# Kernel optimization log

Hardware: AMD Instinct MI355X
Metric: run time of the kernel (lower is better)

Reference implementation:

```python
import jax, jax.numpy as jnp
from jax import lax
import numpy as np

B, D, L = 32, 64, 4096
E = 8          # num_experts
K = 2          # top-k
OC = 32        # out_channels


def setup_inputs() -> dict:
    key = jax.random.key(0)
    ks = jax.random.split(key, 6)
    x = jax.random.normal(ks[0], (B, D, L), dtype=jnp.float32)
    # gating weight [D*5, E] (torch init is zeros; use small random for a meaningful reference)
    w_gate = jax.random.normal(ks[1], (D * 5, E), dtype=jnp.float32) * 0.02
    # Conv1d(D -> OC, kernel 3)
    conv1_w = jax.random.normal(ks[2], (OC, D, 3), dtype=jnp.float32) * (1.0 / np.sqrt(D * 3))
    conv1_b = jax.random.normal(ks[3], (OC,), dtype=jnp.float32) * 0.01
    # Conv1d(OC -> OC*E, kernel 1)
    conv2_w = jax.random.normal(ks[4], (OC * E, OC, 1), dtype=jnp.float32) * (1.0 / np.sqrt(OC))
    conv2_b = jax.random.normal(ks[5], (OC * E,), dtype=jnp.float32) * 0.01
    return {"x": x, "w_gate": w_gate, "conv1_w": conv1_w, "conv1_b": conv1_b,
            "conv2_w": conv2_w, "conv2_b": conv2_b}


def _gates(g_in, w_gate):
    # eval-mode noisy_top_k_gating: no noise, softmax -> top-(k+1) -> renormalize top-k -> scatter
    logits = jax.nn.softmax(g_in @ w_gate, axis=1)            # [B, E]
    top_v, top_i = lax.top_k(logits, min(K + 1, E))           # sorted descending
    vk = top_v[:, :K]
    ik = top_i[:, :K]
    gk = vk / (jnp.sum(vk, axis=1, keepdims=True) + 1e-6)
    gates = jnp.zeros_like(logits).at[jnp.arange(logits.shape[0])[:, None], ik].set(gk)
    return gates


def reference(x, w_gate, conv1_w, conv1_b, conv2_w, conv2_b):
    b, d, l = x.shape
    g_in = x[:, :, -6:-1].reshape(b, d * 5)                   # last-5-timestep gating features
    gates = _gates(g_in, w_gate)                              # [B, E]
    dn = ("NCH", "OIH", "NCH")
    h = lax.conv_general_dilated(x, conv1_w, (1,), "VALID", dimension_numbers=dn)
    h = jnp.tanh(h + conv1_b[None, :, None])                  # [B, OC, L-2]
    out = lax.conv_general_dilated(h, conv2_w, (1,), "VALID", dimension_numbers=dn)
    out = out + conv2_b[None, :, None]                        # [B, OC*E, L']
    lp = out.shape[-1]
    out = out.transpose(0, 2, 1).reshape(b, lp, OC, E)        # [B, L', OC, E]
    moe = jnp.einsum("blde,be->bld", out, gates)              # weighted combine
    return moe.transpose(0, 2, 1)                             # [B, OC, L']
```

## Files before the change

### kernel.cpp

```cpp
#include <hip/hip_runtime.h>
#include <math.h>

#define B_  32
#define D_  64
#define L_  4096
#define E_  8
#define OC_ 32
#define LP_ 4094
#define TILE 128
#define NT   32

typedef __attribute__((ext_vector_type(8)))  short short8;
typedef __attribute__((ext_vector_type(16))) float float16;

static __device__ __forceinline__ unsigned short f2bf(float f) {
    unsigned u = __float_as_uint(f);
    return (unsigned short)((u + 0x7fffu + ((u >> 16) & 1u)) >> 16);
}
static __device__ __forceinline__ unsigned cvtpk(float a, float b) {
    unsigned r;
    asm("v_cvt_pk_bf16_f32 %0, %1, %2" : "=v"(r) : "v"(a), "v"(b));
    return r;
}
static __device__ __forceinline__ float fast_tanh(float x) {
    float e = __expf(2.0f * x);
    return fmaf(-2.0f, __builtin_amdgcn_rcpf(e + 1.0f), 1.0f);
}


__global__ __launch_bounds__(256)
void prep_kernel(const float* __restrict__ x,
                 const float* __restrict__ w_gate,
                 const float* __restrict__ c1w,
                 const float* __restrict__ c2w,
                 const float* __restrict__ c2b,
                 float* __restrict__ beff,
                 unsigned short* __restrict__ aF,
                 unsigned short* __restrict__ wf2)
{
    const int tid = threadIdx.x;

    if (blockIdx.x == 8) {
        for (int i = tid; i < 12 * 64 * 8; i += 256) {
            int ks = i >> 9, lane = (i >> 3) & 63, ii = i & 7;
            int oc = lane & 31, half = lane >> 5;
            int kp = ks * 16 + half * 8 + ii;
            int t = kp >> 6, c = kp & 63;
            aF[i] = f2bf(c1w[oc * 192 + c * 3 + t]);
        }
        return;
    }

    const int wv = tid >> 6, lane = tid & 63;
    const int b  = blockIdx.x * 4 + wv;
    const int d  = lane;

    float xv[5];
    #pragma unroll
    for (int t = 0; t < 5; ++t)
        xv[t] = x[((size_t)b * D_ + d) * L_ + (L_ - 6) + t];

    float part[E_];
    #pragma unroll
    for (int e = 0; e < E_; ++e) part[e] = 0.f;
    #pragma unroll
    for (int t = 0; t < 5; ++t) {
        const float* wg = w_gate + (d * 5 + t) * E_;
        #pragma unroll
        for (int e = 0; e < E_; ++e) part[e] += xv[t] * wg[e];
    }
    #pragma unroll
    for (int off = 1; off < 64; off <<= 1) {
        #pragma unroll
        for (int e = 0; e < E_; ++e)
            part[e] += __shfl_xor(part[e], off, 64);
    }
    float m = part[0];
    #pragma unroll
    for (int e = 1; e < E_; ++e) m = fmaxf(m, part[e]);
    float p[E_], s = 0.f;
    #pragma unroll
    for (int e = 0; e < E_; ++e) { p[e] = expf(part[e] - m); s += p[e]; }
    float inv = 1.f / s;
    #pragma unroll
    for (int e = 0; e < E_; ++e) p[e] *= inv;

    int i0 = 0;
    #pragma unroll
    for (int e = 1; e < E_; ++e) if (p[e] > p[i0]) i0 = e;
    int i1 = (i0 == 0) ? 1 : 0;
    #pragma unroll
    for (int e = 0; e < E_; ++e) {
        if (e == i0) continue;
        if (p[e] > p[i1]) i1 = e;
    }
    const float v0 = p[i0], v1 = p[i1];
    const float den = v0 + v1 + 1e-6f;
    const float g0 = v0 / den, g1 = v1 / den;

    {
        const int dd = lane & 31, half = lane >> 5;
        #pragma unroll
        for (int ks = 0; ks < 2; ++ks) {
            #pragma unroll
            for (int i = 0; i < 8; ++i) {
                int oc = ks * 16 + half * 8 + i;
                float v = g0 * c2w[(dd * E_ + i0) * OC_ + oc]
                        + g1 * c2w[(dd * E_ + i1) * OC_ + oc];
                wf2[((b * 2 + ks) * 64 + lane) * 8 + i] = f2bf(v);
            }
        }
    }
    if (d < OC_)
        beff[b * OC_ + d] = g0 * c2b[d * E_ + i0] + g1 * c2b[d * E_ + i1];
}

__global__ __launch_bounds__(256, 4)
void fused_main(const float* __restrict__ x,
                const unsigned short* __restrict__ aF,
                const unsigned short* __restrict__ wf2,
                const float* __restrict__ beff,
                const float* __restrict__ c1b,
                float* __restrict__ out)
{
    __shared__ __align__(16) unsigned short xT[130 * 64];

    const int tid  = threadIdx.x;
    const int lane = tid & 63;
    const int wv   = tid >> 6;
    const int b    = blockIdx.x >> 5;
    const int l0   = (blockIdx.x & 31) << 7;
    const float* xb = x + (size_t)b * (D_ * L_);

    {
        const int c2 = tid >> 3;
        const int jb = (tid & 7) << 2;
        const float* p0 = xb + (size_t)(2 * c2) * L_ + l0;
        const float* p1 = p0 + L_;
        #pragma unroll
        for (int jq = 0; jq < 4; ++jq) {
            int j = jq * 32 + jb;
            float4 v0 = *(const float4*)(p0 + j);
            float4 v1 = *(const float4*)(p1 + j);
            float e0[4] = {v0.x, v0.y, v0.z, v0.w};
            float e1[4] = {v1.x, v1.y, v1.z, v1.w};
            #pragma unroll
            for (int r = 0; r < 4; ++r) {
                int row = j + r;
                int off = (row * 128 + c2 * 4) ^ ((row & 7) << 4);
                *(unsigned*)((char*)xT + off) = cvtpk(e0[r], e1[r]);
            }
        }
        if (tid < 64) {
            int cc2 = tid >> 1, jj = tid & 1;
            int row = TILE + jj;
            int lg  = l0 + row;
            float f0 = 0.f, f1 = 0.f;
            if (lg < L_) {
                f0 = xb[(size_t)(2 * cc2) * L_ + lg];
                f1 = xb[(size_t)(2 * cc2 + 1) * L_ + lg];
            }
            int off = (row * 128 + cc2 * 4) ^ ((row & 7) << 4);
            *(unsigned*)((char*)xT + off) = cvtpk(f0, f1);
        }
    }

    const int cl = lane & 31;
    const int hi = lane >> 5;

    __syncthreads();

    const int cb = wv * 32;
    float16 acc = (float16)0.0f;
    #pragma unroll
    for (int t = 0; t < 3; ++t) {
        int row = cb + cl + t;
        int rb  = row * 128;
        int swz = (row & 7) << 4;
        #pragma unroll
        for (int q = 0; q < 4; ++q) {
            short8 af = *(const short8*)(aF + ((t * 4 + q) * 64 + lane) * 8);
            int off = (rb + q * 32 + hi * 16) ^ swz;
            short8 bf = *(const short8*)((const char*)xT + off);
            acc = __builtin_amdgcn_mfma_f32_32x32x16_bf16(af, bf, acc, 0, 0, 0);
        }
    }

    short8 a2[2];
    a2[0] = *(const short8*)(wf2 + ((b * 2 + 0) * 64 + lane) * 8);
    a2[1] = *(const short8*)(wf2 + ((b * 2 + 1) * 64 + lane) * 8);

    float th[16];
    #pragma unroll
    for (int r = 0; r < 16; ++r) {
        int row = (r & 3) + 8 * (r >> 2) + 4 * hi;
        th[r] = fast_tanh(acc[r] + c1b[row]);
    }

    unsigned x0a = hi ? cvtpk(th[0],  th[1])  : cvtpk(th[4],  th[5]);
    unsigned x0b = hi ? cvtpk(th[2],  th[3])  : cvtpk(th[6],  th[7]);
    unsigned x1a = hi ? cvtpk(th[8],  th[9])  : cvtpk(th[12], th[13]);
    unsigned x1b = hi ? cvtpk(th[10], th[11]) : cvtpk(th[14], th[15]);
    unsigned r0a = (unsigned)__shfl_xor((int)x0a, 32, 64);
    unsigned r0b = (unsigned)__shfl_xor((int)x0b, 32, 64);
    unsigned r1a = (unsigned)__shfl_xor((int)x1a, 32, 64);
    unsigned r1b = (unsigned)__shfl_xor((int)x1b, 32, 64);

    union U { short8 s8; unsigned u[4]; };
    U b0, b1;
    b0.u[0] = hi ? r0a : cvtpk(th[0], th[1]);
    b0.u[1] = hi ? r0b : cvtpk(th[2], th[3]);
    b0.u[2] = hi ? cvtpk(th[4], th[5]) : r0a;
    b0.u[3] = hi ? cvtpk(th[6], th[7]) : r0b;
    b1.u[0] = hi ? r1a : cvtpk(th[8], th[9]);
    b1.u[1] = hi ? r1b : cvtpk(th[10], th[11]);
    b1.u[2] = hi ? cvtpk(th[12], th[13]) : r1a;
    b1.u[3] = hi ? cvtpk(th[14], th[15]) : r1b;

    float16 acc2 = (float16)0.0f;
    acc2 = __builtin_amdgcn_mfma_f32_32x32x16_bf16(a2[0], b0.s8, acc2, 0, 0, 0);
    acc2 = __builtin_amdgcn_mfma_f32_32x32x16_bf16(a2[1], b1.s8, acc2, 0, 0, 0);

    int l = l0 + cb + cl;
    if (l < LP_) {
        const float* be = beff + b * OC_;
        float* ob = out + (size_t)b * (OC_ * (size_t)LP_) + l;
        #pragma unroll
        for (int r = 0; r < 16; ++r) {
            int row = (r & 3) + 8 * (r >> 2) + 4 * hi;
            ob[(size_t)row * LP_] = acc2[r] + be[row];
        }
    }
}

extern "C" void kernel_launch(void* const* d_in, const int* in_sizes, int n_in,
                              void* d_out, int out_size, void* d_ws, size_t ws_size,
                              hipStream_t stream)
{
    const float* x      = (const float*)d_in[0];
    const float* w_gate = (const float*)d_in[1];
    const float* c1w    = (const float*)d_in[2];
    const float* c1b    = (const float*)d_in[3];
    const float* c2w    = (const float*)d_in[4];
    const float* c2b    = (const float*)d_in[5];
    float* out = (float*)d_out;

    char* ws = (char*)d_ws;
    float* beff         = (float*)ws;
    unsigned short* aF  = (unsigned short*)(ws + 4096);
    unsigned short* wf2 = (unsigned short*)(ws + 16384);

    prep_kernel<<<9, 256, 0, stream>>>(x, w_gate, c1w, c2w, c2b, beff, aF, wf2);
    fused_main<<<B_ * NT, 256, 0, stream>>>(x, aF, wf2, beff, c1b, out);
}
```

Before: 22.00 us.

## Fuse gating and weight-prep kernel into main conv kernel

Removes the separate prep kernel and recomputes, in every block, the gating softmax/top-k, the bf16 packing of conv1 weights into LDS, and the gate-combined conv2 weights and bias. This eliminates one kernel launch and the serialized dependency between the two kernels. In exchange, each of the 1024 blocks redundantly does gating reductions and extra global loads of weights, which adds per-block latency before the MFMA work.

```diff
diff --git a/kernel.cpp b/kernel.cpp
--- a/kernel.cpp
+++ b/kernel.cpp
@@ -13,10 +13,6 @@
 typedef __attribute__((ext_vector_type(8)))  short short8;
 typedef __attribute__((ext_vector_type(16))) float float16;
 
-static __device__ __forceinline__ unsigned short f2bf(float f) {
-    unsigned u = __float_as_uint(f);
-    return (unsigned short)((u + 0x7fffu + ((u >> 16) & 1u)) >> 16);
-}
 static __device__ __forceinline__ unsigned cvtpk(float a, float b) {
     unsigned r;
     asm("v_cvt_pk_bf16_f32 %0, %1, %2" : "=v"(r) : "v"(a), "v"(b));
@@ -27,103 +23,17 @@
     return fmaf(-2.0f, __builtin_amdgcn_rcpf(e + 1.0f), 1.0f);
 }
 
-
-__global__ __launch_bounds__(256)
-void prep_kernel(const float* __restrict__ x,
-                 const float* __restrict__ w_gate,
-                 const float* __restrict__ c1w,
-                 const float* __restrict__ c2w,
-                 const float* __restrict__ c2b,
-                 float* __restrict__ beff,
-                 unsigned short* __restrict__ aF,
-                 unsigned short* __restrict__ wf2)
-{
-    const int tid = threadIdx.x;
-
-    if (blockIdx.x == 8) {
-        for (int i = tid; i < 12 * 64 * 8; i += 256) {
-            int ks = i >> 9, lane = (i >> 3) & 63, ii = i & 7;
-            int oc = lane & 31, half = lane >> 5;
-            int kp = ks * 16 + half * 8 + ii;
-            int t = kp >> 6, c = kp & 63;
-            aF[i] = f2bf(c1w[oc * 192 + c * 3 + t]);
-        }
-        return;
-    }
-
-    const int wv = tid >> 6, lane = tid & 63;
-    const int b  = blockIdx.x * 4 + wv;
-    const int d  = lane;
-
-    float xv[5];
-    #pragma unroll
-    for (int t = 0; t < 5; ++t)
-        xv[t] = x[((size_t)b * D_ + d) * L_ + (L_ - 6) + t];
-
-    float part[E_];
-    #pragma unroll
-    for (int e = 0; e < E_; ++e) part[e] = 0.f;
-    #pragma unroll
-    for (int t = 0; t < 5; ++t) {
-        const float* wg = w_gate + (d * 5 + t) * E_;
-        #pragma unroll
-        for (int e = 0; e < E_; ++e) part[e] += xv[t] * wg[e];
-    }
-    #pragma unroll
-    for (int off = 1; off < 64; off <<= 1) {
-        #pragma unroll
-        for (int e = 0; e < E_; ++e)
-            part[e] += __shfl_xor(part[e], off, 64);
-    }
-    float m = part[0];
-    #pragma unroll
-    for (int e = 1; e < E_; ++e) m = fmaxf(m, part[e]);
-    float p[E_], s = 0.f;
-    #pragma unroll
-    for (int e = 0; e < E_; ++e) { p[e] = expf(part[e] - m); s += p[e]; }
-    float inv = 1.f / s;
-    #pragma unroll
-    for (int e = 0; e < E_; ++e) p[e] *= inv;
-
-    int i0 = 0;
-    #pragma unroll
-    for (int e = 1; e < E_; ++e) if (p[e] > p[i0]) i0 = e;
-    int i1 = (i0 == 0) ? 1 : 0;
-    #pragma unroll
-    for (int e = 0; e < E_; ++e) {
-        if (e == i0) continue;
-        if (p[e] > p[i1]) i1 = e;
-    }
-    const float v0 = p[i0], v1 = p[i1];
-    const float den = v0 + v1 + 1e-6f;
-    const float g0 = v0 / den, g1 = v1 / den;
-
-    {
-        const int dd = lane & 31, half = lane >> 5;
-        #pragma unroll
-        for (int ks = 0; ks < 2; ++ks) {
-            #pragma unroll
-            for (int i = 0; i < 8; ++i) {
-                int oc = ks * 16 + half * 8 + i;
-                float v = g0 * c2w[(dd * E_ + i0) * OC_ + oc]
-                        + g1 * c2w[(dd * E_ + i1) * OC_ + oc];
-                wf2[((b * 2 + ks) * 64 + lane) * 8 + i] = f2bf(v);
-            }
-        }
-    }
-    if (d < OC_)
-        beff[b * OC_ + d] = g0 * c2b[d * E_ + i0] + g1 * c2b[d * E_ + i1];
-}
-
 __global__ __launch_bounds__(256, 4)
-void fused_main(const float* __restrict__ x,
-                const unsigned short* __restrict__ aF,
-                const unsigned short* __restrict__ wf2,
-                const float* __restrict__ beff,
-                const float* __restrict__ c1b,
-                float* __restrict__ out)
+void fused_all(const float* __restrict__ x,
+               const float* __restrict__ w_gate,
+               const float* __restrict__ c1w,
+               const float* __restrict__ c1b,
+               const float* __restrict__ c2w,
+               const float* __restrict__ c2b,
+               float* __restrict__ out)
 {
     __shared__ __align__(16) unsigned short xT[130 * 64];
+    __shared__ __align__(16) unsigned short aFl[12 * 64 * 8];
 
     const int tid  = threadIdx.x;
     const int lane = tid & 63;
@@ -165,8 +75,97 @@
         }
     }
 
+    {
+        const int oc = tid >> 3;
+        const int c0 = (tid & 7) << 3;
+        const float* wp = c1w + oc * 192 + c0 * 3;
+        float v[24];
+        #pragma unroll
+        for (int q = 0; q < 6; ++q)
+            *(float4*)(v + 4 * q) = *(const float4*)(wp + 4 * q);
+        const int ksoff = c0 >> 4;
+        const int half  = (c0 >> 3) & 1;
+        #pragma unroll
+        for (int t = 0; t < 3; ++t) {
+            union { short8 s8; unsigned u[4]; } w8;
+            #pragma unroll
+            for (int jj = 0; jj < 4; ++jj)
+                w8.u[jj] = cvtpk(v[(2 * jj) * 3 + t], v[(2 * jj + 1) * 3 + t]);
+            int base = ((t * 4 + ksoff) * 64 + half * 32 + oc) * 8;
+            *(short8*)(aFl + base) = w8.s8;
+        }
+    }
+
+    int i0, i1;
+    float g0, g1;
+    {
+        const int d = lane;
+        float part[E_];
+        #pragma unroll
+        for (int e = 0; e < E_; ++e) part[e] = 0.f;
+        #pragma unroll
+        for (int t = 0; t < 5; ++t) {
+            float xvt = xb[(size_t)d * L_ + (L_ - 6) + t];
+            const float* wgp = w_gate + (d * 5 + t) * E_;
+            float4 wa = *(const float4*)wgp;
+            float4 wb = *(const float4*)(wgp + 4);
+            part[0] = fmaf(xvt, wa.x, part[0]);
+            part[1] = fmaf(xvt, wa.y, part[1]);
+            part[2] = fmaf(xvt, wa.z, part[2]);
+            part[3] = fmaf(xvt, wa.w, part[3]);
+            part[4] = fmaf(xvt, wb.x, part[4]);
+            part[5] = fmaf(xvt, wb.y, part[5]);
+            part[6] = fmaf(xvt, wb.z, part[6]);
+            part[7] = fmaf(xvt, wb.w, part[7]);
+        }
+        #pragma unroll
+        for (int off = 1; off < 64; off <<= 1) {
+            #pragma unroll
+            for (int e = 0; e < E_; ++e)
+                part[e] += __shfl_xor(part[e], off, 64);
+        }
+        float m = part[0];
+        #pragma unroll
+        for (int e = 1; e < E_; ++e) m = fmaxf(m, part[e]);
+        float p[E_], s = 0.f;
+        #pragma unroll
+        for (int e = 0; e < E_; ++e) { p[e] = expf(part[e] - m); s += p[e]; }
+        float inv = 1.f / s;
+        #pragma unroll
+        for (int e = 0; e < E_; ++e) p[e] *= inv;
+
+        i0 = 0;
+        #pragma unroll
+        for (int e = 1; e < E_; ++e) if (p[e] > p[i0]) i0 = e;
+        i1 = (i0 == 0) ? 1 : 0;
+        #pragma unroll
+        for (int e = 0; e < E_; ++e) {
+            if (e == i0) continue;
+            if (p[e] > p[i1]) i1 = e;
+        }
+        const float v0 = p[i0], v1 = p[i1];
+        const float den = v0 + v1 + 1e-6f;
+        g0 = v0 / den;
+        g1 = v1 / den;
+    }
+
     const int cl = lane & 31;
     const int hi = lane >> 5;
+
+    short8 a2[2];
+    #pragma unroll
+    for (int ks = 0; ks < 2; ++ks) {
+        const float* q0 = c2w + (cl * E_ + i0) * OC_ + ks * 16 + hi * 8;
+        const float* q1 = c2w + (cl * E_ + i1) * OC_ + ks * 16 + hi * 8;
+        float4 u0a = *(const float4*)q0, u0b = *(const float4*)(q0 + 4);
+        float4 u1a = *(const float4*)q1, u1b = *(const float4*)(q1 + 4);
+        union { short8 s8; unsigned u[4]; } f;
+        f.u[0] = cvtpk(fmaf(g0, u0a.x, g1 * u1a.x), fmaf(g0, u0a.y, g1 * u1a.y));
+        f.u[1] = cvtpk(fmaf(g0, u0a.z, g1 * u1a.z), fmaf(g0, u0a.w, g1 * u1a.w));
+        f.u[2] = cvtpk(fmaf(g0, u0b.x, g1 * u1b.x), fmaf(g0, u0b.y, g1 * u1b.y));
+        f.u[3] = cvtpk(fmaf(g0, u0b.z, g1 * u1b.z), fmaf(g0, u0b.w, g1 * u1b.w));
+        a2[ks] = f.s8;
+    }
 
     __syncthreads();
 
@@ -179,16 +178,12 @@
         int swz = (row & 7) << 4;
         #pragma unroll
         for (int q = 0; q < 4; ++q) {
-            short8 af = *(const short8*)(aF + ((t * 4 + q) * 64 + lane) * 8);
+            short8 af = *(const short8*)(aFl + ((t * 4 + q) * 64 + lane) * 8);
             int off = (rb + q * 32 + hi * 16) ^ swz;
             short8 bf = *(const short8*)((const char*)xT + off);
             acc = __builtin_amdgcn_mfma_f32_32x32x16_bf16(af, bf, acc, 0, 0, 0);
         }
     }
-
-    short8 a2[2];
-    a2[0] = *(const short8*)(wf2 + ((b * 2 + 0) * 64 + lane) * 8);
-    a2[1] = *(const short8*)(wf2 + ((b * 2 + 1) * 64 + lane) * 8);
 
     float th[16];
     #pragma unroll
@@ -223,12 +218,12 @@
 
     int l = l0 + cb + cl;
     if (l < LP_) {
-        const float* be = beff + b * OC_;
         float* ob = out + (size_t)b * (OC_ * (size_t)LP_) + l;
         #pragma unroll
         for (int r = 0; r < 16; ++r) {
             int row = (r & 3) + 8 * (r >> 2) + 4 * hi;
-            ob[(size_t)row * LP_] = acc2[r] + be[row];
+            float bb = fmaf(g0, c2b[row * E_ + i0], g1 * c2b[row * E_ + i1]);
+            ob[(size_t)row * LP_] = acc2[r] + bb;
         }
     }
 }
@@ -245,11 +240,5 @@
     const float* c2b    = (const float*)d_in[5];
     float* out = (float*)d_out;
 
-    char* ws = (char*)d_ws;
-    float* beff         = (float*)ws;
-    unsigned short* aF  = (unsigned short*)(ws + 4096);
-    unsigned short* wf2 = (unsigned short*)(ws + 16384);
-
-    prep_kernel<<<9, 256, 0, stream>>>(x, w_gate, c1w, c2w, c2b, beff, aF, wf2);
-    fused_main<<<B_ * NT, 256, 0, stream>>>(x, aF, wf2, beff, c1b, out);
-}
+    fused_all<<<B_ * NT, 256, 0, stream>>>(x, w_gate, c1w, c1b, c2w, c2b, out);
+}
```

After: 22.75 us. +3.4%, slower.

## Load conv input fragments directly from global memory, drop LDS staging

Applied to the files above, without the earlier changes.

The shared-memory transpose tile and its barrier are removed. Each lane now reads its eight channels at three consecutive positions straight from global memory into registers, packs them to bf16 and feeds the MFMAs. This avoids LDS writes and reads and the block-wide sync, at the cost of scalar, less vectorised global loads. Adjacent lanes read overlapping addresses, so the design relies on caches to absorb the threefold reuse. Positions near the end are clamped rather than zero-padded, and the affected outputs are masked at the store.

```diff
diff --git a/kernel.cpp b/kernel.cpp
--- a/kernel.cpp
+++ b/kernel.cpp
@@ -123,8 +123,6 @@
                 const float* __restrict__ c1b,
                 float* __restrict__ out)
 {
-    __shared__ __align__(16) unsigned short xT[130 * 64];
-
     const int tid  = threadIdx.x;
     const int lane = tid & 63;
     const int wv   = tid >> 6;
@@ -132,58 +130,38 @@
     const int l0   = (blockIdx.x & 31) << 7;
     const float* xb = x + (size_t)b * (D_ * L_);
 
-    {
-        const int c2 = tid >> 3;
-        const int jb = (tid & 7) << 2;
-        const float* p0 = xb + (size_t)(2 * c2) * L_ + l0;
-        const float* p1 = p0 + L_;
-        #pragma unroll
-        for (int jq = 0; jq < 4; ++jq) {
-            int j = jq * 32 + jb;
-            float4 v0 = *(const float4*)(p0 + j);
-            float4 v1 = *(const float4*)(p1 + j);
-            float e0[4] = {v0.x, v0.y, v0.z, v0.w};
-            float e1[4] = {v1.x, v1.y, v1.z, v1.w};
-            #pragma unroll
-            for (int r = 0; r < 4; ++r) {
-                int row = j + r;
-                int off = (row * 128 + c2 * 4) ^ ((row & 7) << 4);
-                *(unsigned*)((char*)xT + off) = cvtpk(e0[r], e1[r]);
-            }
-        }
-        if (tid < 64) {
-            int cc2 = tid >> 1, jj = tid & 1;
-            int row = TILE + jj;
-            int lg  = l0 + row;
-            float f0 = 0.f, f1 = 0.f;
-            if (lg < L_) {
-                f0 = xb[(size_t)(2 * cc2) * L_ + lg];
-                f1 = xb[(size_t)(2 * cc2 + 1) * L_ + lg];
-            }
-            int off = (row * 128 + cc2 * 4) ^ ((row & 7) << 4);
-            *(unsigned*)((char*)xT + off) = cvtpk(f0, f1);
-        }
-    }
-
     const int cl = lane & 31;
     const int hi = lane >> 5;
-
-    __syncthreads();
-
     const int cb = wv * 32;
+
+    const int l  = l0 + cb + cl;
+    const int lc = (l > L_ - 3) ? (L_ - 3) : l;
+
     float16 acc = (float16)0.0f;
     #pragma unroll
-    for (int t = 0; t < 3; ++t) {
-        int row = cb + cl + t;
-        int rb  = row * 128;
-        int swz = (row & 7) << 4;
-        #pragma unroll
-        for (int q = 0; q < 4; ++q) {
-            short8 af = *(const short8*)(aF + ((t * 4 + q) * 64 + lane) * 8);
-            int off = (rb + q * 32 + hi * 16) ^ swz;
-            short8 bf = *(const short8*)((const char*)xT + off);
-            acc = __builtin_amdgcn_mfma_f32_32x32x16_bf16(af, bf, acc, 0, 0, 0);
-        }
+    for (int q = 0; q < 4; ++q) {
+        const float* xc = xb + (size_t)(q * 16 + hi * 8) * L_ + lc;
+        float v0[8], v1[8], v2[8];
+        #pragma unroll
+        for (int i = 0; i < 8; ++i) {
+            const float* p = xc + (size_t)i * L_;
+            v0[i] = p[0];
+            v1[i] = p[1];
+            v2[i] = p[2];
+        }
+        short8 a0 = *(const short8*)(aF + ((0 * 4 + q) * 64 + lane) * 8);
+        short8 a1 = *(const short8*)(aF + ((1 * 4 + q) * 64 + lane) * 8);
+        short8 a2t = *(const short8*)(aF + ((2 * 4 + q) * 64 + lane) * 8);
+        union { short8 s8; unsigned u[4]; } f0, f1, f2;
+        #pragma unroll
+        for (int j = 0; j < 4; ++j) {
+            f0.u[j] = cvtpk(v0[2 * j], v0[2 * j + 1]);
+            f1.u[j] = cvtpk(v1[2 * j], v1[2 * j + 1]);
+            f2.u[j] = cvtpk(v2[2 * j], v2[2 * j + 1]);
+        }
+        acc = __builtin_amdgcn_mfma_f32_32x32x16_bf16(a0,  f0.s8, acc, 0, 0, 0);
+        acc = __builtin_amdgcn_mfma_f32_32x32x16_bf16(a1,  f1.s8, acc, 0, 0, 0);
+        acc = __builtin_amdgcn_mfma_f32_32x32x16_bf16(a2t, f2.s8, acc, 0, 0, 0);
     }
 
     short8 a2[2];
@@ -221,7 +199,6 @@
     acc2 = __builtin_amdgcn_mfma_f32_32x32x16_bf16(a2[0], b0.s8, acc2, 0, 0, 0);
     acc2 = __builtin_amdgcn_mfma_f32_32x32x16_bf16(a2[1], b1.s8, acc2, 0, 0, 0);
 
-    int l = l0 + cb + cl;
     if (l < LP_) {
         const float* be = beff + b * OC_;
         float* ob = out + (size_t)b * (OC_ * (size_t)LP_) + l;
```

After: 23.56 us. 7.1% more time.
